# Kernel optimization log

Hardware: AMD Instinct MI355X
Metric: run time of the kernel (lower is better)

Reference implementation:

```python
import jax, jax.numpy as jnp
import numpy as np

B, N, K = 16, 2048, 16        # events, nodes per event, neighbors
F_IN, L = 64, 64              # in_size, layer_size
EPS = 1e-5                    # BatchNorm1d eps


def setup_inputs() -> dict:
    key = jax.random.key(0)
    k1, k2 = jax.random.split(key, 2)
    x = jax.random.normal(k1, (B * N, F_IN), jnp.float32)
    batch = jnp.repeat(jnp.arange(B, dtype=jnp.int32), N)  # equal-size events
    W = jax.random.normal(k2, (2 * F_IN, L), jnp.float32) * 0.08
    b = jnp.zeros((L,), jnp.float32)
    gamma = jnp.ones((L,), jnp.float32)
    beta = jnp.zeros((L,), jnp.float32)
    return {"x": x, "batch": batch, "W": W, "b": b, "gamma": gamma, "beta": beta}


def reference(x, batch, W, b, gamma, beta):
    # batch encodes B equal-size events -> reshape to [B, N, F]
    xr = x.reshape(B, N, F_IN)

    # dynamic kNN in feature space, per event (self included, as in PyG knn)
    sq = jnp.sum(xr * xr, axis=-1)                                  # [B, N]
    d = sq[:, :, None] + sq[:, None, :] - 2.0 * jnp.einsum(
        'bnf,bmf->bnm', xr, xr)                                     # [B, N, N]
    _, idx = jax.lax.top_k(-d, K)                                   # [B, N, K]

    # gather neighbor features
    xj = jax.vmap(lambda xe, ie: xe[ie])(xr, idx)                   # [B, N, K, F]
    xi = jnp.broadcast_to(xr[:, :, None, :], (B, N, K, F_IN))

    # EdgeConv message: nn(cat([x_i, x_j - x_i]))
    e = jnp.concatenate([xi, xj - xi], axis=-1)                     # [B, N, K, 2F]
    h = jnp.einsum('bnke,el->bnkl', e, W) + b                       # Linear

    # BatchNorm1d over all edges (training-mode batch stats, biased var)
    m = jnp.mean(h, axis=(0, 1, 2))
    v = jnp.var(h, axis=(0, 1, 2))
    h = (h - m) * jax.lax.rsqrt(v + EPS) * gamma + beta
    h = jax.nn.relu(h)

    # aggr='mean' over the K neighbors
    out = jnp.mean(h, axis=2)                                       # [B, N, L]
    return out.reshape(B * N, L)
```

## Files before the change

kernel.cpp:

```cpp
#include <hip/hip_runtime.h>
#include <hip/hip_fp16.h>
#include <math.h>

#define B_EV    16
#define N_NODES 2048
#define K_NN    16
#define F_IN    64
#define L_OUT   64
#define NT      (B_EV * N_NODES)
#define EDGES   (NT * K_NN)

typedef __attribute__((ext_vector_type(8)))  short bh8;
typedef __attribute__((ext_vector_type(16))) float f32x16;
typedef __attribute__((ext_vector_type(8)))  unsigned short us8;

__device__ inline unsigned short bf16_rne(float f) {
  unsigned int u = __float_as_uint(f);
  return (unsigned short)((u + 0x7FFFu + ((u >> 16) & 1u)) >> 16);
}
__device__ inline float bf16f(unsigned short h) {
  return __uint_as_float(((unsigned int)h) << 16);
}

__device__ inline void gload16(const void* g, void* l) {
  __builtin_amdgcn_global_load_lds(
      (const __attribute__((address_space(1))) void*)(g),
      (__attribute__((address_space(3))) void*)(l), 16, 0, 0);
}

__global__ __launch_bounds__(256) void k_uv(const float* __restrict__ x,
                                            const float* __restrict__ W,
                                            float* __restrict__ u,
                                            float* __restrict__ v,
                                            float* __restrict__ sq,
                                            unsigned short* __restrict__ xh,
                                            unsigned short* __restrict__ xl) {
  __shared__ float xs[64][64];
  const int t = threadIdx.x;
  const int l = t & 63, g = t >> 6;
  const int nodeBase = blockIdx.x * 64;

  {
    const float4* gx = (const float4*)(x + (size_t)nodeBase * 64);
    float4* lx = (float4*)&xs[0][0];
    #pragma unroll
    for (int p = 0; p < 4; ++p) lx[p * 256 + t] = gx[p * 256 + t];
  }
  float wdc[64], w2c[64];
  #pragma unroll
  for (int f = 0; f < 64; ++f) {
    float w1v = W[f * 64 + l];
    float w2v = W[4096 + f * 64 + l];
    wdc[f] = w1v - w2v;
    w2c[f] = w2v;
  }
  __syncthreads();

  #pragma unroll
  for (int p = 0; p < 2; ++p) {
    int n = p * 32 + (t >> 3), j = t & 7;
    float xv = xs[n][j];
    float s = __fmul_rn(xv, xv);
    #pragma unroll
    for (int i = 1; i < 8; ++i) {
      float c = xs[n][j + 8 * i];
      s = __fadd_rn(s, __fmul_rn(c, c));
    }
    s = __fadd_rn(s, __shfl_xor(s, 1));
    s = __fadd_rn(s, __shfl_xor(s, 2));
    s = __fadd_rn(s, __shfl_xor(s, 4));
    if (j == 0) sq[nodeBase + n] = s;
  }
  #pragma unroll
  for (int p = 0; p < 4; ++p) {
    int i = p * 256 + t;
    float4 vv = ((const float4*)&xs[0][0])[i];
    ushort4 h, lo;
    h.x = bf16_rne(vv.x); lo.x = bf16_rne(vv.x - bf16f(h.x));
    h.y = bf16_rne(vv.y); lo.y = bf16_rne(vv.y - bf16f(h.y));
    h.z = bf16_rne(vv.z); lo.z = bf16_rne(vv.z - bf16f(h.z));
    h.w = bf16_rne(vv.w); lo.w = bf16_rne(vv.w - bf16f(h.w));
    ((ushort4*)xh)[(size_t)nodeBase * 16 + i] = h;
    ((ushort4*)xl)[(size_t)nodeBase * 16 + i] = lo;
  }

  for (int rep = 0; rep < 16; ++rep) {
    int n = rep * 4 + g;
    const float4* xr = (const float4*)xs[n];
    float au = 0.f, av = 0.f;
    #pragma unroll
    for (int fq = 0; fq < 16; ++fq) {
      float4 xv = xr[fq];
      au = fmaf(xv.x, wdc[fq * 4 + 0], au); av = fmaf(xv.x, w2c[fq * 4 + 0], av);
      au = fmaf(xv.y, wdc[fq * 4 + 1], au); av = fmaf(xv.y, w2c[fq * 4 + 1], av);
      au = fmaf(xv.z, wdc[fq * 4 + 2], au); av = fmaf(xv.z, w2c[fq * 4 + 2], av);
      au = fmaf(xv.w, wdc[fq * 4 + 3], au); av = fmaf(xv.w, w2c[fq * 4 + 3], av);
    }
    u[(size_t)(nodeBase + n) * 64 + l] = au;
    v[(size_t)(nodeBase + n) * 64 + l] = av;
  }
}

__global__ __launch_bounds__(256, 6) void k_gemm(const unsigned short* __restrict__ xh,
                                                 const unsigned short* __restrict__ xl,
                                                 const float* __restrict__ sq,
                                                 unsigned short* __restrict__ Sbuf,
                                                 int evBase) {
  __shared__ char xb[16384];
  __shared__ __align__(16) unsigned short Sh[32 * 128];
  const int t    = threadIdx.x;
  const int w    = t >> 6;
  const int lane = t & 63;
  const int ev    = evBase + (blockIdx.x >> 6);
  const int strip = blockIdx.x & 63;
  const int rowBase = strip * 32;
  const size_t evNode = (size_t)ev * N_NODES;
  const float* __restrict__ sqev = sq + evNode;
  unsigned short* __restrict__ Sev =
      Sbuf + (size_t)(ev - evBase) * N_NODES * N_NODES;
  char* Sc = (char*)Sh;

  {
    int col = t >> 3;
    int fbs = ((t & 7) << 4) ^ ((col & 7) << 4);
    gload16((const char*)(xh + (evNode + rowBase + col) * 64) + fbs, Sc + t * 16);
    gload16((const char*)(xl + (evNode + rowBase + col) * 64) + fbs, Sc + 4096 + t * 16);
    #pragma unroll
    for (int p = 0; p < 4; ++p) {
      const int colB = p * 32 + (t >> 3);
      const char* g = (const char*)(xh + (evNode + colB) * 64) + fbs;
      gload16(g, xb + p * 4096 + t * 16);
    }
  }
  __syncthreads();
  bh8 ah[4], al[4];
  {
    int row = lane & 31;
    int fb  = (lane >> 5) * 16;
    #pragma unroll
    for (int ks = 0; ks < 4; ++ks) {
      int off = (row * 128 + ks * 32 + fb) ^ ((row & 7) << 4);
      ah[ks] = *(const bh8*)(Sc + off);
      al[ks] = *(const bh8*)(Sc + 4096 + off);
    }
  }
  __syncthreads();

  for (int T = 0; T < 16; ++T) {
    const int tileCol = T * 128;
    {
      f32x16 acc;
      #pragma unroll
      for (int q = 0; q < 16; ++q) acc[q] = 0.f;
      int colIn = w * 32 + (lane & 31);
      int fb = (lane >> 5) * 16;
      #pragma unroll
      for (int ks = 0; ks < 4; ++ks) {
        int off = (colIn * 128 + ks * 32 + fb) ^ ((colIn & 7) << 4);
        bh8 bh = *(const bh8*)(xb + off);
        acc = __builtin_amdgcn_mfma_f32_32x32x16_bf16(ah[ks], bh, acc, 0, 0, 0);
        acc = __builtin_amdgcn_mfma_f32_32x32x16_bf16(al[ks], bh, acc, 0, 0, 0);
      }
      float sqc = sqev[tileCol + colIn];
      #pragma unroll
      for (int reg = 0; reg < 16; ++reg) {
        int m = (reg & 3) + 8 * (reg >> 2) + 4 * (lane >> 5);
        Sh[m * 128 + colIn] =
            __half_as_ushort(__float2half(fmaf(-2.0f, acc[reg], sqc)));
      }
    }
    __syncthreads();
    if (T < 15) {
      #pragma unroll
      for (int p = 0; p < 4; ++p) {
        const int colB = p * 32 + (t >> 3);
        const int fbs = ((t & 7) << 4) ^ (((t >> 3) & 7) << 4);
        const char* g = (const char*)(xh + (evNode + tileCol + 128 + colB) * 64) + fbs;
        gload16(g, xb + p * 4096 + t * 16);
      }
    }
    {
      int r  = t >> 3;
      int cg = t & 7;
      unsigned short* gS =
          Sev + (size_t)(rowBase + r) * N_NODES + tileCol + cg * 16;
      const uint4* lS = (const uint4*)(Sh + r * 128 + cg * 16);
      *(uint4*)gS = lS[0];
      *(uint4*)(gS + 8) = lS[1];
    }
    __syncthreads();
  }
}

#define SCR_CAP 192
#define SEL_DELTA 1.0f

__global__ __launch_bounds__(256, 8) void k_scr(const unsigned short* __restrict__ Sbuf,
                                                int* __restrict__ cand,
                                                int* __restrict__ cnt,
                                                int rowBase) {
  const int w = threadIdx.x >> 6, lane = threadIdx.x & 63;
  const int rowInChunk = blockIdx.x * 4 + w;
  const int grow = rowBase + rowInChunk;
  const unsigned short* __restrict__ Srow = Sbuf + (size_t)rowInChunk * N_NODES;

  us8 pk[4];
  #pragma unroll
  for (int q = 0; q < 4; ++q)
    pk[q] = *(const us8*)(Srow + q * 512 + lane * 8);

  float mn = 3.4e38f;
  #pragma unroll
  for (int q = 0; q < 4; ++q) {
    #pragma unroll
    for (int e = 0; e < 8; ++e)
      mn = fminf(mn, __half2float(__ushort_as_half(pk[q][e])));
  }
  #pragma unroll
  for (int k = 2; k <= 64; k <<= 1) {
    #pragma unroll
    for (int j = k >> 1; j >= 1; j >>= 1) {
      float o = __shfl_xor(mn, j);
      bool up = ((lane & k) == 0);
      bool iAmLower = ((lane & j) == 0);
      bool wantSmall = (up == iAmLower);
      bool less = (mn < o);
      if (less != wantSmall) mn = o;
    }
  }
  const float thr = __shfl(mn, 15) + SEL_DELTA;

  unsigned int msk[4];
  int c = 0;
  #pragma unroll
  for (int q = 0; q < 4; ++q) {
    unsigned int m = 0;
    #pragma unroll
    for (int e = 0; e < 8; ++e) {
      float v = __half2float(__ushort_as_half(pk[q][e]));
      m |= (v <= thr) ? (1u << e) : 0u;
    }
    msk[q] = m;
    c += __popc(m);
  }
  int incl = c;
  #pragma unroll
  for (int off = 1; off < 64; off <<= 1) {
    int n = __shfl_up(incl, off);
    if (lane >= off) incl += n;
  }
  int pos = incl - c;
  int total = __shfl(incl, 63);
  if (lane == 0) cnt[grow] = (total < SCR_CAP) ? total : SCR_CAP;
  int* crow = cand + (size_t)grow * SCR_CAP;
  #pragma unroll
  for (int q = 0; q < 4; ++q) {
    unsigned int m = msk[q];
    while (m) {
      int e = __ffs(m) - 1;
      m &= m - 1;
      if (pos < SCR_CAP) crow[pos] = q * 512 + lane * 8 + e;
      ++pos;
    }
  }
}

__global__ __launch_bounds__(256, 1) void k_resc(const float* __restrict__ x,
                                                 const float* __restrict__ sq,
                                                 const int* __restrict__ cand,
                                                 const int* __restrict__ cnt,
                                                 int* __restrict__ nidx,
                                                 int rowBase) {
  __shared__ float xiS[4][64];
  __shared__ unsigned long long keysLDS[4][SCR_CAP];
  const int w = threadIdx.x >> 6, lane = threadIdx.x & 63;
  const int grow = rowBase + blockIdx.x * 4 + w;
  const int ev = grow >> 11;
  const int rowInEv = grow & 2047;
  const size_t evNode = (size_t)ev * N_NODES;
  const float* __restrict__ sqev = sq + evNode;
  const int cn = cnt[grow];
  const int* __restrict__ crow = cand + (size_t)grow * SCR_CAP;
  const float* __restrict__ xev = x + evNode * F_IN;

  xiS[w][lane] = x[(evNode + rowInEv) * F_IN + lane];
  __syncthreads();

  const float sqn = sqev[rowInEv];
  const float* xiW = xiS[w];

  int base = 0;
  while (base < cn) {
    int rem = cn - base;
    if (rem <= 32) {
      int hf = lane >> 5;
      int ii = lane & 31;
      int ci = base + ii;
      bool act = ii < rem;
      int mcol = act ? crow[ci] : 0;
      const float4* xm = (const float4*)(xev + (size_t)mcol * F_IN);
      double d0 = 0.0, d1 = 0.0;
      #pragma unroll
      for (int q = 0; q < 8; ++q) {
        int fq = hf * 8 + q;
        float4 cc = xm[fq];
        float4 xq = *(const float4*)(xiW + fq * 4);
        d0 = fma((double)xq.x, (double)cc.x, d0);
        d1 = fma((double)xq.y, (double)cc.y, d1);
        d0 = fma((double)xq.z, (double)cc.z, d0);
        d1 = fma((double)xq.w, (double)cc.w, d1);
      }
      double ds = d0 + d1;
      double od = __shfl_xor(ds, 32);
      if (act && hf == 0) {
        float dot32 = (float)(ds + od);
        float sv = __fsub_rn(__fadd_rn(sqn, sqev[mcol]), __fmul_rn(2.0f, dot32));
        unsigned int fb = __float_as_uint(sv);
        fb = (fb & 0x80000000u) ? ~fb : (fb | 0x80000000u);
        keysLDS[w][ci] = ((unsigned long long)fb << 32) | (unsigned int)mcol;
      }
      base = cn;
    } else {
      int ci = base + lane;
      bool act = ci < cn;
      int mcol = act ? crow[ci] : 0;
      const float4* xm = (const float4*)(xev + (size_t)mcol * F_IN);
      double d0 = 0.0, d1 = 0.0, d2 = 0.0, d3 = 0.0;
      #pragma unroll
      for (int fq = 0; fq < 16; fq += 4) {
        float4 c0 = xm[fq + 0], c1 = xm[fq + 1], c2 = xm[fq + 2], c3 = xm[fq + 3];
        float4 x0 = *(const float4*)(xiW + fq * 4);
        float4 x1 = *(const float4*)(xiW + fq * 4 + 4);
        float4 x2 = *(const float4*)(xiW + fq * 4 + 8);
        float4 x3 = *(const float4*)(xiW + fq * 4 + 12);
        d0 = fma((double)x0.x, (double)c0.x, d0);
        d0 = fma((double)x0.y, (double)c0.y, d0);
        d0 = fma((double)x0.z, (double)c0.z, d0);
        d0 = fma((double)x0.w, (double)c0.w, d0);
        d1 = fma((double)x1.x, (double)c1.x, d1);
        d1 = fma((double)x1.y, (double)c1.y, d1);
        d1 = fma((double)x1.z, (double)c1.z, d1);
        d1 = fma((double)x1.w, (double)c1.w, d1);
        d2 = fma((double)x2.x, (double)c2.x, d2);
        d2 = fma((double)x2.y, (double)c2.y, d2);
        d2 = fma((double)x2.z, (double)c2.z, d2);
        d2 = fma((double)x2.w, (double)c2.w, d2);
        d3 = fma((double)x3.x, (double)c3.x, d3);
        d3 = fma((double)x3.y, (double)c3.y, d3);
        d3 = fma((double)x3.z, (double)c3.z, d3);
        d3 = fma((double)x3.w, (double)c3.w, d3);
      }
      if (act) {
        float dot32 = (float)((d0 + d1) + (d2 + d3));
        float sv = __fsub_rn(__fadd_rn(sqn, sqev[mcol]), __fmul_rn(2.0f, dot32));
        unsigned int fb = __float_as_uint(sv);
        fb = (fb & 0x80000000u) ? ~fb : (fb | 0x80000000u);
        keysLDS[w][ci] = ((unsigned long long)fb << 32) | (unsigned int)mcol;
      }
      base += 64;
    }
  }
  __syncthreads();

  const unsigned long long INVALID = ~0ull;
  unsigned long long k0 = INVALID, k1 = INVALID, k2 = INVALID;
  if (lane < cn)        k0 = keysLDS[w][lane];
  if (lane + 64 < cn)   k1 = keysLDS[w][lane + 64];
  if (lane + 128 < cn)  k2 = keysLDS[w][lane + 128];
  int r0 = 0, r1 = 0, r2 = 0;
  for (int i = 0; i < cn; ++i) {
    unsigned long long kk = keysLDS[w][i];
    r0 += (kk < k0) ? 1 : 0;
    r1 += (kk < k1) ? 1 : 0;
    r2 += (kk < k2) ? 1 : 0;
  }
  const size_t outBase = (evNode + rowInEv) * K_NN;
  if (lane < cn && r0 < K_NN)
    nidx[outBase + r0] = (int)evNode + (int)(k0 & 0x7FFFFFFFu);
  if (lane + 64 < cn && r1 < K_NN)
    nidx[outBase + r1] = (int)evNode + (int)(k1 & 0x7FFFFFFFu);
  if (lane + 128 < cn && r2 < K_NN)
    nidx[outBase + r2] = (int)evNode + (int)(k2 & 0x7FFFFFFFu);
}

#define NS 16
#define NC 128
union KnnSmem {
  struct {
    char  xb[32768];
    float S[32 * 129];
  } a;
  struct {
    float sc[32][NC + 1];
    int   id[32][NC + 1];
    int   cand[32][24];
    float resc[32][24];
  } b;
};

__global__ __launch_bounds__(256, 3) void k_knn(const float* __restrict__ x,
                                                const unsigned short* __restrict__ xh,
                                                const unsigned short* __restrict__ xl,
                                                const float* __restrict__ sq,
                                                int* __restrict__ nidx) {
  __shared__ KnnSmem sm;
  const int t    = threadIdx.x;
  const int r    = t & 31;
  const int c8   = t >> 5;
  const int w    = t >> 6;
  const int lane = t & 63;
  const int ev    = blockIdx.x >> 6;
  const int strip = blockIdx.x & 63;
  const int rowBase = strip * 32;
  const size_t evNode = (size_t)ev * N_NODES;
  const float* __restrict__ sqev = sq + evNode;

  {
    int col = t >> 3;
    int fb  = (t & 7) << 4;
    const char* gh = (const char*)(xh + (evNode + rowBase + col) * 64) + fb;
    const char* gl = (const char*)(xl + (evNode + rowBase + col) * 64) + fb;
    int off = (col * 128 + fb) ^ ((col & 7) << 4);
    *(uint4*)(sm.a.xb + off)         = *(const uint4*)gh;
    *(uint4*)(sm.a.xb + 16384 + off) = *(const uint4*)gl;
  }
  __syncthreads();
  bh8 ah[4], al[4];
  {
    int row = lane & 31;
    int fb  = (lane >> 5) * 16;
    #pragma unroll
    for (int ks = 0; ks < 4; ++ks) {
      int off = (row * 128 + ks * 32 + fb) ^ ((row & 7) << 4);
      ah[ks] = *(const bh8*)(sm.a.xb + off);
      al[ks] = *(const bh8*)(sm.a.xb + 16384 + off);
    }
  }

  float dist[NS]; int idxk[NS];
  #pragma unroll
  for (int q = 0; q < NS; ++q) { dist[q] = 3.4e38f; idxk[q] = 0x7FFFFFFF; }
  float curMax = 3.4e38f;

  for (int T = 0; T < 16; ++T) {
    __syncthreads();
    const int tileCol = T * 128;
    #pragma unroll
    for (int p = 0; p < 8; ++p) {
      int idx16 = (p & 3) * 256 + t;
      int col = idx16 >> 3;
      int fb  = (idx16 & 7) << 4;
      const unsigned short* src = (p < 4) ? xh : xl;
      const char* g = (const char*)(src + (evNode + tileCol + col) * 64) + fb;
      int off = ((p < 4) ? 0 : 16384) + ((col * 128 + fb) ^ ((col & 7) << 4));
      *(uint4*)(sm.a.xb + off) = *(const uint4*)g;
    }
    __syncthreads();
    {
      f32x16 acc;
      #pragma unroll
      for (int q = 0; q < 16; ++q) acc[q] = 0.f;
      int colIn = w * 32 + (lane & 31);
      int fb = (lane >> 5) * 16;
      #pragma unroll
      for (int ks = 0; ks < 4; ++ks) {
        int off = (colIn * 128 + ks * 32 + fb) ^ ((colIn & 7) << 4);
        bh8 bh = *(const bh8*)(sm.a.xb + off);
        bh8 bl = *(const bh8*)(sm.a.xb + 16384 + off);
        acc = __builtin_amdgcn_mfma_f32_32x32x16_bf16(ah[ks], bh, acc, 0, 0, 0);
        acc = __builtin_amdgcn_mfma_f32_32x32x16_bf16(ah[ks], bl, acc, 0, 0, 0);
        acc = __builtin_amdgcn_mfma_f32_32x32x16_bf16(al[ks], bh, acc, 0, 0, 0);
      }
      float sqc = sqev[tileCol + colIn];
      #pragma unroll
      for (int reg = 0; reg < 16; ++reg) {
        int m = (reg & 3) + 8 * (reg >> 2) + 4 * (lane >> 5);
        sm.a.S[m * 129 + colIn] = fmaf(-2.0f, acc[reg], sqc);
      }
    }
    __syncthreads();
    for (int j = 0; j < 16; ++j) {
      int cIn = c8 * 16 + j;
      float s = sm.a.S[r * 129 + cIn];
      if (s <= curMax) {
        int col = tileCol + cIn;
        float bv = dist[0]; int bi = idxk[0]; int slot = 0;
        #pragma unroll
        for (int q = 1; q < NS; ++q) {
          bool worse = (dist[q] > bv) || ((dist[q] == bv) && (idxk[q] > bi));
          slot = worse ? q : slot;
          bv = worse ? dist[q] : bv;
          bi = worse ? idxk[q] : bi;
        }
        if ((s < bv) || ((s == bv) && (col < bi))) {
          #pragma unroll
          for (int q = 0; q < NS; ++q) {
            dist[q] = (q == slot) ? s : dist[q];
            idxk[q] = (q == slot) ? col : idxk[q];
          }
          float cm = dist[0];
          #pragma unroll
          for (int q = 1; q < NS; ++q) cm = fmaxf(cm, dist[q]);
          curMax = cm;
        }
      }
    }
  }

  __syncthreads();
  #pragma unroll
  for (int q = 0; q < NS; ++q) {
    sm.b.sc[r][c8 * NS + q] = dist[q];
    sm.b.id[r][c8 * NS + q] = idxk[q];
  }
  __syncthreads();

  if (t < 32) {
    float dd[24]; int di[24];
    #pragma unroll
    for (int q = 0; q < 24; ++q) { dd[q] = 3.4e38f; di[q] = 0x7FFFFFFF; }
    for (int c = 0; c < NC; ++c) {
      float s = sm.b.sc[t][c];
      int m = sm.b.id[t][c];
      float bv = dd[0]; int bi = di[0]; int slot = 0;
      #pragma unroll
      for (int q = 1; q < 24; ++q) {
        bool worse = (dd[q] > bv) || ((dd[q] == bv) && (di[q] > bi));
        slot = worse ? q : slot;
        bv = worse ? dd[q] : bv;
        bi = worse ? di[q] : bi;
      }
      if ((s < bv) || ((s == bv) && (m < bi))) {
        #pragma unroll
        for (int q = 0; q < 24; ++q) {
          dd[q] = (q == slot) ? s : dd[q];
          di[q] = (q == slot) ? m : di[q];
        }
      }
    }
    #pragma unroll
    for (int q = 0; q < 24; ++q) sm.b.cand[t][q] = di[q];
  }
  __syncthreads();

  {
    float4 xi[16];
    const float4* xr = (const float4*)(x + (evNode + rowBase + r) * F_IN);
    #pragma unroll
    for (int fq = 0; fq < 16; ++fq) xi[fq] = xr[fq];
    const float sqn = sqev[rowBase + r];
    const float* __restrict__ xev = x + evNode * F_IN;
    #pragma unroll
    for (int ii = 0; ii < 3; ++ii) {
      int i = c8 + ii * 8;
      int m = sm.b.cand[r][i];
      const float4* xm = (const float4*)(xev + (size_t)m * F_IN);
      double dot = 0.0;
      #pragma unroll
      for (int fq = 0; fq < 16; ++fq) {
        float4 cc = xm[fq];
        dot = fma((double)xi[fq].x, (double)cc.x, dot);
        dot = fma((double)xi[fq].y, (double)cc.y, dot);
        dot = fma((double)xi[fq].z, (double)cc.z, dot);
        dot = fma((double)xi[fq].w, (double)cc.w, dot);
      }
      const float dot32 = (float)dot;
      sm.b.resc[r][i] = __fsub_rn(__fadd_rn(sqn, sqev[m]),
                                  __fmul_rn(2.0f, dot32));
    }
  }
  __syncthreads();

  if (t < 32) {
    float dd[K_NN]; int di[K_NN];
    #pragma unroll
    for (int q = 0; q < K_NN; ++q) { dd[q] = 3.4e38f; di[q] = 0x7FFFFFFF; }
    for (int c = 0; c < 24; ++c) {
      float s = sm.b.resc[t][c];
      int m = sm.b.cand[t][c];
      float bv = dd[0]; int bi = di[0]; int slot = 0;
      #pragma unroll
      for (int q = 1; q < K_NN; ++q) {
        bool worse = (dd[q] > bv) || ((dd[q] == bv) && (di[q] > bi));
        slot = worse ? q : slot;
        bv = worse ? dd[q] : bv;
        bi = worse ? di[q] : bi;
      }
      if ((s < bv) || ((s == bv) && (m < bi))) {
        #pragma unroll
        for (int q = 0; q < K_NN; ++q) {
          dd[q] = (q == slot) ? s : dd[q];
          di[q] = (q == slot) ? m : di[q];
        }
      }
    }
    const size_t row = evNode + rowBase + t;
    #pragma unroll
    for (int q = 0; q < K_NN; ++q)
      nidx[row * K_NN + q] = (int)evNode + di[q];
  }
}

#define NB_ST 32
__global__ __launch_bounds__(256) void k_stats(const float* __restrict__ u,
                                               const float* __restrict__ v,
                                               const int* __restrict__ nidx,
                                               const float* __restrict__ bvec,
                                               float* __restrict__ stats) {
  __shared__ float red1[4][64];
  __shared__ float red2[4][64];
  const int l = threadIdx.x & 63, g = threadIdx.x >> 6;
  const int base = blockIdx.x * NB_ST;
  const float bl = bvec[l];
  float s1 = 0.f, s2 = 0.f;
  for (int nn = g; nn < NB_ST; nn += 4) {
    const int node = base + nn;
    const float ui = u[(size_t)node * 64 + l] + bl;
    const int* ip = nidx + (size_t)node * K_NN;
    int idx[16];
    #pragma unroll
    for (int q = 0; q < 4; ++q)
      *(int4*)&idx[q * 4] = *(const int4*)(ip + q * 4);
    #pragma unroll
    for (int k = 0; k < K_NN; ++k) {
      const float vj = v[(size_t)idx[k] * 64 + l];
      const float h = ui + vj;
      s1 += h;
      s2 = fmaf(h, h, s2);
    }
  }
  red1[g][l] = s1; red2[g][l] = s2;
  __syncthreads();
  if (g == 0) {
    float t1 = red1[0][l] + red1[1][l] + red1[2][l] + red1[3][l];
    float t2 = red2[0][l] + red2[1][l] + red2[2][l] + red2[3][l];
    atomicAdd(&stats[l], t1);
    atomicAdd(&stats[64 + l], t2);
  }
}

__global__ __launch_bounds__(256) void k_out(const float* __restrict__ u,
                                             const float* __restrict__ v,
                                             const int* __restrict__ nidx,
                                             const float* __restrict__ bvec,
                                             const float* __restrict__ gamma,
                                             const float* __restrict__ beta,
                                             const float* __restrict__ stats,
                                             float* __restrict__ out) {
  const int l = threadIdx.x & 63, g = threadIdx.x >> 6;
  const float inv = 1.0f / (float)EDGES;
  const float mean = stats[l] * inv;
  const float ex2 = stats[64 + l] * inv;
  const float var = ex2 - mean * mean;
  const float a = gamma[l] * rsqrtf(var + 1e-5f);
  const float bb = fmaf(-mean, a, beta[l]);
  const float bl = bvec[l];
  const int base = blockIdx.x * NB_ST;
  for (int nn = g; nn < NB_ST; nn += 4) {
    const int node = base + nn;
    const float ui = u[(size_t)node * 64 + l] + bl;
    const int* ip = nidx + (size_t)node * K_NN;
    int idx[16];
    #pragma unroll
    for (int q = 0; q < 4; ++q)
      *(int4*)&idx[q * 4] = *(const int4*)(ip + q * 4);
    float acc = 0.f;
    #pragma unroll
    for (int k = 0; k < K_NN; ++k) {
      const float vj = v[(size_t)idx[k] * 64 + l];
      const float h = ui + vj;
      acc += fmaxf(fmaf(a, h, bb), 0.f);
    }
    out[(size_t)node * 64 + l] = acc * (1.0f / 16.0f);
  }
}

extern "C" void kernel_launch(void* const* d_in, const int* in_sizes, int n_in,
                              void* d_out, int out_size, void* d_ws, size_t ws_size,
                              hipStream_t stream) {
  (void)in_sizes; (void)n_in; (void)out_size;
  const float* x     = (const float*)d_in[0];
  const float* W     = (const float*)d_in[2];
  const float* b     = (const float*)d_in[3];
  const float* gamma = (const float*)d_in[4];
  const float* beta  = (const float*)d_in[5];
  float* out = (float*)d_out;

  char* ws = (char*)d_ws;
  float*          u     = (float*)(ws);
  float*          v     = (float*)(ws + 8388608);
  float*          sq    = (float*)(ws + 16777216);
  int*            nidx  = (int*)  (ws + 16908288);
  float*          stats = (float*)(ws + 19005440);
  unsigned short* xh    = (unsigned short*)(ws + 19005952);
  unsigned short* xl    = (unsigned short*)(ws + 23200256);
  int*            cnt   = (int*)  (ws + 27394560);
  int*            cand  = (int*)  (ws + 27525632);
  unsigned short* Sbuf  = (unsigned short*)(ws + 52691456);

  const size_t sChunkBytes = (size_t)N_NODES * N_NODES * 2;
  size_t avail = (ws_size > 52691456) ? ws_size - 52691456 : 0;
  int evCap = (int)((avail / sChunkBytes < 16) ? (avail / sChunkBytes) : 16);

  hipMemsetAsync(stats, 0, 512, stream);
  k_uv  <<<512, 256, 0, stream>>>(x, W, u, v, sq, xh, xl);

  if (evCap >= 1) {
    for (int e0 = 0; e0 < B_EV; e0 += evCap) {
      int ne = (B_EV - e0 < evCap) ? (B_EV - e0) : evCap;
      k_gemm<<<ne * 64, 256, 0, stream>>>(xh, xl, sq, Sbuf, e0);
      k_scr <<<ne * 512, 256, 0, stream>>>(Sbuf, cand, cnt, e0 * N_NODES);
      k_resc<<<ne * 512, 256, 0, stream>>>(x, sq, cand, cnt, nidx, e0 * N_NODES);
    }
  } else {
    k_knn<<<1024, 256, 0, stream>>>(x, xh, xl, sq, nidx);
  }

  k_stats<<<1024, 256, 0, stream>>>(u, v, nidx, b, stats);
  k_out <<<1024, 256, 0, stream>>>(u, v, nidx, b, gamma, beta, stats, out);
}
```

Measured before the change: 179.7 us.

## Fuse screening and rescoring kernels; split distance GEMM strips across two blocks

The screening and exact-rescoring kernels are merged into one k_sel kernel, so candidate lists stay in LDS instead of going out to global cand/cnt arrays and being read back. The __syncthreads calls between phases are removed because each wave works only on its own row. Separately, each k_gemm block now covers half the column tiles, doubling the grid for more parallelism at the cost of loading the A strip twice. The fused kernel keeps launch_bounds(256,1) and uses more LDS, which may limit occupancy during the screening phase.

Result: faster. 174.0 us (-3.2%).

```diff
diff --git a/kernel.cpp b/kernel.cpp
--- a/kernel.cpp
+++ b/kernel.cpp
@@ -111,9 +111,12 @@
   const int t    = threadIdx.x;
   const int w    = t >> 6;
   const int lane = t & 63;
-  const int ev    = evBase + (blockIdx.x >> 6);
-  const int strip = blockIdx.x & 63;
+  const int ev    = evBase + (blockIdx.x >> 7);
+  const int rem   = blockIdx.x & 127;
+  const int strip = rem >> 1;
+  const int half  = rem & 1;
   const int rowBase = strip * 32;
+  const int T0 = half * 8;
   const size_t evNode = (size_t)ev * N_NODES;
   const float* __restrict__ sqev = sq + evNode;
   unsigned short* __restrict__ Sev =
@@ -128,7 +131,7 @@
     #pragma unroll
     for (int p = 0; p < 4; ++p) {
       const int colB = p * 32 + (t >> 3);
-      const char* g = (const char*)(xh + (evNode + colB) * 64) + fbs;
+      const char* g = (const char*)(xh + (evNode + T0 * 128 + colB) * 64) + fbs;
       gload16(g, xb + p * 4096 + t * 16);
     }
   }
@@ -146,7 +149,7 @@
   }
   __syncthreads();
 
-  for (int T = 0; T < 16; ++T) {
+  for (int T = T0; T < T0 + 8; ++T) {
     const int tileCol = T * 128;
     {
       f32x16 acc;
@@ -170,7 +173,7 @@
       }
     }
     __syncthreads();
-    if (T < 15) {
+    if (T < T0 + 7) {
       #pragma unroll
       for (int p = 0; p < 4; ++p) {
         const int colB = p * 32 + (t >> 3);
@@ -195,14 +198,25 @@
 #define SCR_CAP 192
 #define SEL_DELTA 1.0f
 
-__global__ __launch_bounds__(256, 8) void k_scr(const unsigned short* __restrict__ Sbuf,
-                                                int* __restrict__ cand,
-                                                int* __restrict__ cnt,
+__global__ __launch_bounds__(256, 1) void k_sel(const float* __restrict__ x,
+                                                const float* __restrict__ sq,
+                                                const unsigned short* __restrict__ Sbuf,
+                                                int* __restrict__ nidx,
                                                 int rowBase) {
+  __shared__ float xiS[4][64];
+  __shared__ int candLDS[4][SCR_CAP];
+  __shared__ unsigned long long keysLDS[4][SCR_CAP];
   const int w = threadIdx.x >> 6, lane = threadIdx.x & 63;
   const int rowInChunk = blockIdx.x * 4 + w;
   const int grow = rowBase + rowInChunk;
+  const int ev = grow >> 11;
+  const int rowInEv = grow & 2047;
+  const size_t evNode = (size_t)ev * N_NODES;
   const unsigned short* __restrict__ Srow = Sbuf + (size_t)rowInChunk * N_NODES;
+  const float* __restrict__ sqev = sq + evNode;
+  const float* __restrict__ xev = x + evNode * F_IN;
+
+  xiS[w][lane] = x[(evNode + rowInEv) * F_IN + lane];
 
   us8 pk[4];
   #pragma unroll
@@ -251,43 +265,21 @@
   }
   int pos = incl - c;
   int total = __shfl(incl, 63);
-  if (lane == 0) cnt[grow] = (total < SCR_CAP) ? total : SCR_CAP;
-  int* crow = cand + (size_t)grow * SCR_CAP;
+  const int cn = (total < SCR_CAP) ? total : SCR_CAP;
   #pragma unroll
   for (int q = 0; q < 4; ++q) {
     unsigned int m = msk[q];
     while (m) {
       int e = __ffs(m) - 1;
       m &= m - 1;
-      if (pos < SCR_CAP) crow[pos] = q * 512 + lane * 8 + e;
+      if (pos < SCR_CAP) candLDS[w][pos] = q * 512 + lane * 8 + e;
       ++pos;
     }
   }
-}
-
-__global__ __launch_bounds__(256, 1) void k_resc(const float* __restrict__ x,
-                                                 const float* __restrict__ sq,
-                                                 const int* __restrict__ cand,
-                                                 const int* __restrict__ cnt,
-                                                 int* __restrict__ nidx,
-                                                 int rowBase) {
-  __shared__ float xiS[4][64];
-  __shared__ unsigned long long keysLDS[4][SCR_CAP];
-  const int w = threadIdx.x >> 6, lane = threadIdx.x & 63;
-  const int grow = rowBase + blockIdx.x * 4 + w;
-  const int ev = grow >> 11;
-  const int rowInEv = grow & 2047;
-  const size_t evNode = (size_t)ev * N_NODES;
-  const float* __restrict__ sqev = sq + evNode;
-  const int cn = cnt[grow];
-  const int* __restrict__ crow = cand + (size_t)grow * SCR_CAP;
-  const float* __restrict__ xev = x + evNode * F_IN;
-
-  xiS[w][lane] = x[(evNode + rowInEv) * F_IN + lane];
-  __syncthreads();
 
   const float sqn = sqev[rowInEv];
   const float* xiW = xiS[w];
+  const int* crow = candLDS[w];
 
   int base = 0;
   while (base < cn) {
@@ -360,7 +352,6 @@
       base += 64;
     }
   }
-  __syncthreads();
 
   const unsigned long long INVALID = ~0ull;
   unsigned long long k0 = INVALID, k1 = INVALID, k2 = INVALID;
@@ -694,12 +685,10 @@
   float*          stats = (float*)(ws + 19005440);
   unsigned short* xh    = (unsigned short*)(ws + 19005952);
   unsigned short* xl    = (unsigned short*)(ws + 23200256);
-  int*            cnt   = (int*)  (ws + 27394560);
-  int*            cand  = (int*)  (ws + 27525632);
-  unsigned short* Sbuf  = (unsigned short*)(ws + 52691456);
+  unsigned short* Sbuf  = (unsigned short*)(ws + 27394560);
 
   const size_t sChunkBytes = (size_t)N_NODES * N_NODES * 2;
-  size_t avail = (ws_size > 52691456) ? ws_size - 52691456 : 0;
+  size_t avail = (ws_size > 27394560) ? ws_size - 27394560 : 0;
   int evCap = (int)((avail / sChunkBytes < 16) ? (avail / sChunkBytes) : 16);
 
   hipMemsetAsync(stats, 0, 512, stream);
@@ -708,9 +697,8 @@
   if (evCap >= 1) {
     for (int e0 = 0; e0 < B_EV; e0 += evCap) {
       int ne = (B_EV - e0 < evCap) ? (B_EV - e0) : evCap;
-      k_gemm<<<ne * 64, 256, 0, stream>>>(xh, xl, sq, Sbuf, e0);
-      k_scr <<<ne * 512, 256, 0, stream>>>(Sbuf, cand, cnt, e0 * N_NODES);
-      k_resc<<<ne * 512, 256, 0, stream>>>(x, sq, cand, cnt, nidx, e0 * N_NODES);
+      k_gemm<<<ne * 128, 256, 0, stream>>>(xh, xl, sq, Sbuf, e0);
+      k_sel <<<ne * 512, 256, 0, stream>>>(x, sq, Sbuf, nidx, e0 * N_NODES);
     }
   } else {
     k_knn<<<1024, 256, 0, stream>>>(x, xh, xl, sq, nidx);
```
